# Optimization experiments

Hardware: AMD Instinct MI355X
Metric: run time of the kernel (lower is better)

## Reference

```python
import jax, jax.numpy as jnp
import numpy as np

N_NODES = 100000
N_EDGES = 3200000
N_GRAPHS = 256


def setup_inputs() -> dict:
    key = jax.random.key(0)
    ks = jax.random.split(key, 8)
    x = jax.random.normal(ks[0], (N_NODES, 13), dtype=jnp.float32)
    edge_index = jax.random.randint(ks[1], (2, N_EDGES), 0, N_NODES, dtype=jnp.int64)
    batch = jnp.sort(jax.random.randint(ks[2], (N_NODES,), 0, N_GRAPHS, dtype=jnp.int64))
    W1 = jax.random.normal(ks[3], (13, 64), dtype=jnp.float32) * 0.1
    b1 = jnp.zeros((64,), dtype=jnp.float32)
    W2 = jax.random.normal(ks[4], (64, 64), dtype=jnp.float32) * 0.1
    b2 = jnp.zeros((64,), dtype=jnp.float32)
    W3 = jax.random.normal(ks[5], (64, 32), dtype=jnp.float32) * 0.1
    b3 = jnp.zeros((32,), dtype=jnp.float32)
    return {"x": x, "edge_index": edge_index, "batch": batch,
            "W1": W1, "b1": b1, "W2": W2, "b2": b2, "W3": W3, "b3": b3}


def _gcn_norm(edge_index, num_nodes):
    # PyG GCNConv default: add self-loops, symmetric D^-1/2 (A+I) D^-1/2 normalization.
    loops = jnp.arange(num_nodes, dtype=edge_index.dtype)
    src = jnp.concatenate([edge_index[0], loops])
    dst = jnp.concatenate([edge_index[1], loops])
    ones = jnp.ones(src.shape[0], dtype=jnp.float32)
    deg = jax.ops.segment_sum(ones, dst, num_segments=num_nodes)
    dinv = jnp.where(deg > 0, jax.lax.rsqrt(deg), 0.0)
    norm = dinv[src] * dinv[dst]  # [E+N]
    return src, dst, norm


def _gcn_conv(h, W, b, src, dst, norm, num_nodes):
    h = h @ W                                   # [N, out]
    msg = h[src] * norm[:, None]                # gather + scale, [E+N, out]
    out = jax.ops.segment_sum(msg, dst, num_segments=num_nodes)  # scatter-add
    return out + b


def reference(x, edge_index, batch, W1, b1, W2, b2, W3, b3):
    n = x.shape[0]
    src, dst, norm = _gcn_norm(edge_index, n)
    h = jax.nn.relu(_gcn_conv(x, W1, b1, src, dst, norm, n))
    h = jax.nn.relu(_gcn_conv(h, W2, b2, src, dst, norm, n))
    h = _gcn_conv(h, W3, b3, src, dst, norm, n)
    # global_mean_pool over graphs
    sums = jax.ops.segment_sum(h, batch, num_segments=N_GRAPHS)
    counts = jax.ops.segment_sum(jnp.ones((n,), jnp.float32), batch, num_segments=N_GRAPHS)
    return sums / jnp.maximum(counts, 1.0)[:, None]
```

## Files before the change

### kernel.cpp

```cpp
#include <hip/hip_runtime.h>
#include <hip/hip_fp16.h>

constexpr int NN = 100000;
constexpr int NE = 3200000;
constexpr int NG = 256;
constexpr int NCB = 196;
constexpr int TILE = 4096;
constexpr int EPT = TILE / 256;
constexpr int CAP = 17408;

__global__ void k_zero_i(int* __restrict__ p, int n) {
  int i = blockIdx.x * blockDim.x + threadIdx.x;
  if (i < n) p[i] = 0;
}

__global__ void k_msplit(const int* __restrict__ src, const int* __restrict__ dst,
                         int* __restrict__ gcursor, int* __restrict__ pairs, int E) {
  constexpr int NT = 256;
  __shared__ int hist[NCB], lbase[NCB], lcur[NCB], gwrite[NCB];
  __shared__ int staged[TILE];
  __shared__ unsigned char sbid[TILE];
  __shared__ int stot;
  const int tid = threadIdx.x;
  const int e0 = blockIdx.x * TILE;
  for (int i = tid; i < NCB; i += NT) { hist[i] = 0; lcur[i] = 0; }
  __syncthreads();
  int4 ls[EPT / 4], ld[EPT / 4];
  bool valid[EPT / 4];
#pragma unroll
  for (int j = 0; j < EPT / 4; ++j) {
    int e = e0 + j * (NT * 4) + tid * 4;
    valid[j] = (e < E);
    if (valid[j]) {
      ls[j] = *(const int4*)(src + e);
      ld[j] = *(const int4*)(dst + e);
      atomicAdd(&hist[ld[j].x >> 9], 1);
      atomicAdd(&hist[ld[j].y >> 9], 1);
      atomicAdd(&hist[ld[j].z >> 9], 1);
      atomicAdd(&hist[ld[j].w >> 9], 1);
    }
  }
  __syncthreads();
  if (tid == 0) {
    int run = 0;
    for (int c = 0; c < NCB; ++c) { lbase[c] = run; run += hist[c]; }
    stot = run;
  }
  __syncthreads();
  for (int c = tid; c < NCB; c += NT) {
    int cnt = hist[c];
    if (cnt > 0) {
      int g = atomicAdd(&gcursor[c], cnt);
      gwrite[c] = c * CAP + g;
    }
  }
  __syncthreads();
#pragma unroll
  for (int j = 0; j < EPT / 4; ++j) {
    if (valid[j]) {
      int ss[4] = {ls[j].x, ls[j].y, ls[j].z, ls[j].w};
      int dd[4] = {ld[j].x, ld[j].y, ld[j].z, ld[j].w};
#pragma unroll
      for (int q = 0; q < 4; ++q) {
        int c = dd[q] >> 9;
        int pos = lbase[c] + atomicAdd(&lcur[c], 1);
        staged[pos] = ss[q] | ((dd[q] & 511) << 17);
        sbid[pos] = (unsigned char)c;
      }
    }
  }
  __syncthreads();
  const int total = stot;
  for (int i = tid; i < total; i += NT) {
    int c = sbid[i];
    pairs[gwrite[c] + (i - lbase[c])] = staged[i];
  }
}

__global__ void k_brow(const int* __restrict__ pairs, const int* __restrict__ gcursor,
                       int* __restrict__ rowstart, float* __restrict__ dinv,
                       int* __restrict__ csr_src) {
  __shared__ int deg[512], pre[512], cur[512];
  __shared__ int s[256];
  const int cb = blockIdx.x;
  const int n0 = cb << 9;
  const int tid = threadIdx.x;
  s[tid] = (tid < NCB) ? gcursor[tid] : 0;
  __syncthreads();
  for (int o = 1; o < 256; o <<= 1) {
    int v = s[tid];
    int u = (tid >= o) ? s[tid - o] : 0;
    __syncthreads();
    s[tid] = v + u;
    __syncthreads();
  }
  const int e0 = (cb == 0) ? 0 : s[cb - 1];
  const int cnt = gcursor[cb];
  const int p0 = cb * CAP;
  __syncthreads();
  for (int i = tid; i < 512; i += 256) { deg[i] = 0; cur[i] = 0; }
  __syncthreads();
  for (int e = tid; e < cnt; e += 256) atomicAdd(&deg[pairs[p0 + e] >> 17], 1);
  __syncthreads();
  int d0 = deg[2 * tid], d1 = deg[2 * tid + 1];
  s[tid] = d0 + d1;
  __syncthreads();
  for (int o = 1; o < 256; o <<= 1) {
    int v = s[tid];
    int u = (tid >= o) ? s[tid - o] : 0;
    __syncthreads();
    s[tid] = v + u;
    __syncthreads();
  }
  int p2 = (tid == 0) ? 0 : s[tid - 1];
  pre[2 * tid] = p2;
  pre[2 * tid + 1] = p2 + d0;
  __syncthreads();
  for (int i = tid; i < 512; i += 256) {
    int n = n0 + i;
    if (n < NN) {
      rowstart[n] = e0 + pre[i];
      dinv[n] = rsqrtf((float)(deg[i] + 1));
    }
  }
  if (cb == NCB - 1 && tid == 0) rowstart[NN] = NE;
  for (int e = tid; e < cnt; e += 256) {
    int w = pairs[p0 + e];
    int dl = w >> 17;
    int p = e0 + pre[dl] + atomicAdd(&cur[dl], 1);
    csr_src[p] = w & 0x1FFFF;
  }
}

__global__ void k_xs(const float* __restrict__ x, const float* __restrict__ dinv,
                     __half* __restrict__ xs) {
  int i = blockIdx.x * blockDim.x + threadIdx.x;
  if (i < NN * 16) {
    int v = i >> 4, f = i & 15;
    float val = (f < 13) ? x[v * 13 + f] * dinv[v] : 0.0f;
    xs[i] = __float2half_rn(val);
  }
}

__global__ void __launch_bounds__(256) k_l1fused(
    const __half* __restrict__ xs, const int* __restrict__ rowstart,
    const int* __restrict__ csr_src, const float* __restrict__ dinv,
    const float* __restrict__ W1, const float* __restrict__ b1,
    const float* __restrict__ W2, __half* __restrict__ t2) {
  __shared__ float W1s[13 * 64];
  __shared__ float B1s[64];
  __shared__ float W2s[64 * 64];
  __shared__ float aggs[4][16];
  __shared__ float h1s[4][64];
  __shared__ int lidx[4][64];
  const int tid = threadIdx.x;
  for (int i = tid; i < 13 * 64; i += 256) W1s[i] = W1[i];
  if (tid < 64) B1s[tid] = b1[tid];
  for (int i = tid; i < 64 * 64; i += 256) W2s[i] = W2[i];
  __syncthreads();
  const int wv = tid >> 6;
  const int lane = tid & 63;
  const int node = blockIdx.x * 4 + wv;
  const int fp = lane & 7;
  const int es = lane >> 3;
  const __half2* x2 = (const __half2*)xs;
  const int r0 = rowstart[node], r1 = rowstart[node + 1];
  float ax = 0.0f, ay = 0.0f;
  if (es == 0) {
    float2 sf = __half22float2(x2[node * 8 + fp]);
    ax = sf.x; ay = sf.y;
  }
  for (int base = r0; base < r1; base += 64) {
    const int nc = min(64, r1 - base);
    lidx[wv][lane] = (base + lane < r1) ? csr_src[base + lane] : 0;
    int i = es;
    for (; i + 24 < nc; i += 32) {
      int s0 = lidx[wv][i], s1 = lidx[wv][i + 8], s2 = lidx[wv][i + 16], s3 = lidx[wv][i + 24];
      float2 v0 = __half22float2(x2[s0 * 8 + fp]);
      float2 v1 = __half22float2(x2[s1 * 8 + fp]);
      float2 v2 = __half22float2(x2[s2 * 8 + fp]);
      float2 v3 = __half22float2(x2[s3 * 8 + fp]);
      ax += (v0.x + v1.x) + (v2.x + v3.x);
      ay += (v0.y + v1.y) + (v2.y + v3.y);
    }
    for (; i < nc; i += 8) {
      int s = lidx[wv][i];
      float2 v = __half22float2(x2[s * 8 + fp]);
      ax += v.x; ay += v.y;
    }
  }
  ax += __shfl_xor(ax, 32); ay += __shfl_xor(ay, 32);
  ax += __shfl_xor(ax, 16); ay += __shfl_xor(ay, 16);
  ax += __shfl_xor(ax, 8);  ay += __shfl_xor(ay, 8);
  const float di = dinv[node];
  if (lane < 8) {
    aggs[wv][2 * fp]     = ax * di;
    aggs[wv][2 * fp + 1] = ay * di;
  }
  float acc = B1s[lane];
#pragma unroll
  for (int k = 0; k < 13; ++k) acc += aggs[wv][k] * W1s[k * 64 + lane];
  h1s[wv][lane] = fmaxf(acc, 0.0f);
  float a2 = 0.0f;
#pragma unroll
  for (int k = 0; k < 64; ++k) a2 += h1s[wv][k] * W2s[k * 64 + lane];
  t2[node * 64 + lane] = __float2half_rn(a2 * di);
}

__global__ void __launch_bounds__(256) k_gather64m(
    const __half* __restrict__ t, const int* __restrict__ rowstart,
    const int* __restrict__ csr_src, const float* __restrict__ dinv,
    const float* __restrict__ b2, const float* __restrict__ W3,
    __half* __restrict__ t3) {
  __shared__ float W3s[64 * 32];
  __shared__ float h2s[4][64];
  __shared__ int lidx[4][64];
  const int tid = threadIdx.x;
  for (int i = tid; i < 64 * 32; i += 256) W3s[i] = W3[i];
  __syncthreads();
  const int w = tid >> 6;
  const int lane = tid & 63;
  const int node = blockIdx.x * 4 + w;
  const int fp = lane & 31;
  const int es = lane >> 5;
  const __half2* t2 = (const __half2*)t;
  const int r0 = rowstart[node], r1 = rowstart[node + 1];
  float ax = 0.0f, ay = 0.0f;
  if (es == 0) {
    float2 sf = __half22float2(t2[node * 32 + fp]);
    ax = sf.x; ay = sf.y;
  }
  for (int base = r0; base < r1; base += 64) {
    const int nc = min(64, r1 - base);
    lidx[w][lane] = (base + lane < r1) ? csr_src[base + lane] : 0;
    int i = es;
    for (; i + 14 < nc; i += 16) {
      int s0 = lidx[w][i],      s1 = lidx[w][i + 2],  s2 = lidx[w][i + 4],  s3 = lidx[w][i + 6];
      int s4 = lidx[w][i + 8],  s5 = lidx[w][i + 10], s6 = lidx[w][i + 12], s7 = lidx[w][i + 14];
      float2 v0 = __half22float2(t2[s0 * 32 + fp]);
      float2 v1 = __half22float2(t2[s1 * 32 + fp]);
      float2 v2 = __half22float2(t2[s2 * 32 + fp]);
      float2 v3 = __half22float2(t2[s3 * 32 + fp]);
      float2 v4 = __half22float2(t2[s4 * 32 + fp]);
      float2 v5 = __half22float2(t2[s5 * 32 + fp]);
      float2 v6 = __half22float2(t2[s6 * 32 + fp]);
      float2 v7 = __half22float2(t2[s7 * 32 + fp]);
      ax += ((v0.x + v1.x) + (v2.x + v3.x)) + ((v4.x + v5.x) + (v6.x + v7.x));
      ay += ((v0.y + v1.y) + (v2.y + v3.y)) + ((v4.y + v5.y) + (v6.y + v7.y));
    }
    for (; i < nc; i += 2) {
      int s = lidx[w][i];
      float2 v = __half22float2(t2[s * 32 + fp]);
      ax += v.x; ay += v.y;
    }
  }
  ax += __shfl_xor(ax, 32); ay += __shfl_xor(ay, 32);
  const float di = dinv[node];
  if (es == 0) {
    float2 bb = ((const float2*)b2)[fp];
    h2s[w][2 * fp]     = fmaxf(ax * di + bb.x, 0.0f);
    h2s[w][2 * fp + 1] = fmaxf(ay * di + bb.y, 0.0f);
  }
  const int j = lane & 31, kh = lane >> 5;
  float p = 0.0f;
#pragma unroll
  for (int k2 = 0; k2 < 32; ++k2) {
    int k = kh * 32 + k2;
    p += h2s[w][k] * W3s[k * 32 + j];
  }
  p += __shfl_xor(p, 32);
  if (lane < 32) t3[node * 32 + j] = __float2half_rn(p * di);
}

__global__ void k_gather32w(const __half* __restrict__ t, const int* __restrict__ rowstart,
                            const int* __restrict__ csr_src,
                            const float* __restrict__ dinv, const float* __restrict__ b,
                            __half* __restrict__ h3) {
  __shared__ int lidx[4][64];
  const int wv = threadIdx.x >> 6;
  const int node = (blockIdx.x * blockDim.x + threadIdx.x) >> 6;
  const int lane = threadIdx.x & 63;
  const int fp = lane & 15;
  const int es = lane >> 4;
  const __half2* t2 = (const __half2*)t;
  const int r0 = rowstart[node], r1 = rowstart[node + 1];
  float ax = 0.0f, ay = 0.0f;
  if (es == 0) {
    float2 sf = __half22float2(t2[node * 16 + fp]);
    ax = sf.x; ay = sf.y;
  }
  for (int base = r0; base < r1; base += 64) {
    const int nc = min(64, r1 - base);
    lidx[wv][lane] = (base + lane < r1) ? csr_src[base + lane] : 0;
    int i = es;
    for (; i + 28 < nc; i += 32) {
      int s0 = lidx[wv][i],      s1 = lidx[wv][i + 4],  s2 = lidx[wv][i + 8],  s3 = lidx[wv][i + 12];
      int s4 = lidx[wv][i + 16], s5 = lidx[wv][i + 20], s6 = lidx[wv][i + 24], s7 = lidx[wv][i + 28];
      float2 v0 = __half22float2(t2[s0 * 16 + fp]);
      float2 v1 = __half22float2(t2[s1 * 16 + fp]);
      float2 v2 = __half22float2(t2[s2 * 16 + fp]);
      float2 v3 = __half22float2(t2[s3 * 16 + fp]);
      float2 v4 = __half22float2(t2[s4 * 16 + fp]);
      float2 v5 = __half22float2(t2[s5 * 16 + fp]);
      float2 v6 = __half22float2(t2[s6 * 16 + fp]);
      float2 v7 = __half22float2(t2[s7 * 16 + fp]);
      ax += ((v0.x + v1.x) + (v2.x + v3.x)) + ((v4.x + v5.x) + (v6.x + v7.x));
      ay += ((v0.y + v1.y) + (v2.y + v3.y)) + ((v4.y + v5.y) + (v6.y + v7.y));
    }
    for (; i < nc; i += 4) {
      int s = lidx[wv][i];
      float2 v = __half22float2(t2[s * 16 + fp]);
      ax += v.x; ay += v.y;
    }
  }
  ax += __shfl_xor(ax, 32); ay += __shfl_xor(ay, 32);
  ax += __shfl_xor(ax, 16); ay += __shfl_xor(ay, 16);
  if (lane < 16) {
    const float di = dinv[node];
    float2 bb = ((const float2*)b)[fp];
    ((__half2*)h3)[node * 16 + fp] = __floats2half2_rn(ax * di + bb.x, ay * di + bb.y);
  }
}

__global__ void k_pool(const __half* __restrict__ h3, const int* __restrict__ batch,
                       float* __restrict__ out) {
  const int g = blockIdx.x;
  int lo = 0, hi = NN;
  while (lo < hi) { int m = (lo + hi) >> 1; if (batch[m] < g) lo = m + 1; else hi = m; }
  const int a = lo;
  lo = 0; hi = NN;
  while (lo < hi) { int m = (lo + hi) >> 1; if (batch[m] < g + 1) lo = m + 1; else hi = m; }
  const int bEnd = lo;
  const int tid = threadIdx.x;
  const int nl = tid >> 4, f = tid & 15;
  const __half2* h2p = (const __half2*)h3;
  float ax = 0.0f, ay = 0.0f;
  for (int n = a + nl; n < bEnd; n += 16) {
    float2 v = __half22float2(h2p[n * 16 + f]);
    ax += v.x; ay += v.y;
  }
  __shared__ float redx[16][16], redy[16][16];
  redx[nl][f] = ax; redy[nl][f] = ay;
  __syncthreads();
  if (tid < 16) {
    float sx = 0.0f, sy = 0.0f;
#pragma unroll
    for (int i = 0; i < 16; ++i) { sx += redx[i][tid]; sy += redy[i][tid]; }
    float inv = 1.0f / fmaxf((float)(bEnd - a), 1.0f);
    ((float2*)out)[g * 16 + tid] = make_float2(sx * inv, sy * inv);
  }
}

extern "C" void kernel_launch(void* const* d_in, const int* in_sizes, int n_in,
                              void* d_out, int out_size, void* d_ws, size_t ws_size,
                              hipStream_t stream) {
  const float* x  = (const float*)d_in[0];
  const int*   ei = (const int*)d_in[1];
  const int* batch = (const int*)d_in[2];
  const float* W1 = (const float*)d_in[3];
  const float* b1 = (const float*)d_in[4];
  const float* W2 = (const float*)d_in[5];
  const float* b2 = (const float*)d_in[6];
  const float* W3 = (const float*)d_in[7];
  const float* b3 = (const float*)d_in[8];
  float* out = (float*)d_out;

  const int* src = ei;
  const int* dst = ei + NE;

  float* ws = (float*)d_ws;
  float* dinv     = ws;
  int*   gcursor  = (int*)(ws + 100352);
  int*   rowstart = (int*)(ws + 100944);
  int*   csr_src  = (int*)(ws + 201056);
  float* bufT     = ws + 3401056;
  float* bufH     = ws + 9801056;
  int*    pairs = (int*)bufT;
  __half* t2    = (__half*)bufT;
  __half* h3    = (__half*)(bufT + 1600000);
  __half* xs    = (__half*)bufH;
  __half* t3    = (__half*)bufH;

  const int B = 256;
  auto cdiv = [](int a, int b) { return (a + b - 1) / b; };

  k_zero_i<<<1, B, 0, stream>>>(gcursor, NCB);
  k_msplit<<<cdiv(NE, TILE), B, 0, stream>>>(src, dst, gcursor, pairs, NE);
  k_brow<<<NCB, B, 0, stream>>>(pairs, gcursor, rowstart, dinv, csr_src);

  k_xs<<<cdiv(NN * 16, B), B, 0, stream>>>(x, dinv, xs);
  k_l1fused<<<NN / 4, B, 0, stream>>>(xs, rowstart, csr_src, dinv, W1, b1, W2, t2);

  k_gather64m<<<NN / 4, B, 0, stream>>>(t2, rowstart, csr_src, dinv, b2, W3, t3);

  k_gather32w<<<cdiv(NN * 64, B), B, 0, stream>>>(t3, rowstart, csr_src, dinv, b3, h3);
  k_pool<<<NG, B, 0, stream>>>(h3, batch, out);
}
```

Measured before the change: 319.9 us.

## Make layer-1 fused kernel persistent with W2 held in registers

The layer-1 gather+MLP kernel becomes a grid-stride persistent kernel with 1024 blocks instead of one block per 4 nodes. Each thread now keeps a 16x4 slice of W2 in registers, loaded once per block. The 64x64 matvec is split over four lane groups and reduced with cross-lane shuffles. This removes the per-block 16KB staging of W2 into shared memory repeated across 25000 blocks. The trade-off is higher register pressure, which may lower occupancy, and extra shuffle work per node.

```diff
diff --git a/kernel.cpp b/kernel.cpp
--- a/kernel.cpp
+++ b/kernel.cpp
@@ -8,6 +8,8 @@
 constexpr int TILE = 4096;
 constexpr int EPT = TILE / 256;
 constexpr int CAP = 17408;
+constexpr int L1_BLOCKS = 1024;
+constexpr int L1_WAVES = L1_BLOCKS * 4;
 
 __global__ void k_zero_i(int* __restrict__ p, int n) {
   int i = blockIdx.x * blockDim.x + threadIdx.x;
@@ -142,69 +144,89 @@
   }
 }
 
-__global__ void __launch_bounds__(256) k_l1fused(
+__global__ void __launch_bounds__(256, 4) k_l1fused(
     const __half* __restrict__ xs, const int* __restrict__ rowstart,
     const int* __restrict__ csr_src, const float* __restrict__ dinv,
     const float* __restrict__ W1, const float* __restrict__ b1,
     const float* __restrict__ W2, __half* __restrict__ t2) {
   __shared__ float W1s[13 * 64];
   __shared__ float B1s[64];
-  __shared__ float W2s[64 * 64];
   __shared__ float aggs[4][16];
   __shared__ float h1s[4][64];
   __shared__ int lidx[4][64];
   const int tid = threadIdx.x;
   for (int i = tid; i < 13 * 64; i += 256) W1s[i] = W1[i];
   if (tid < 64) B1s[tid] = b1[tid];
-  for (int i = tid; i < 64 * 64; i += 256) W2s[i] = W2[i];
-  __syncthreads();
   const int wv = tid >> 6;
   const int lane = tid & 63;
-  const int node = blockIdx.x * 4 + wv;
+  const int c4 = lane & 15, kh = lane >> 4;
+  float w2r[16][4];
+#pragma unroll
+  for (int i = 0; i < 16; ++i) {
+    float4 v = *(const float4*)(W2 + (kh * 16 + i) * 64 + c4 * 4);
+    w2r[i][0] = v.x; w2r[i][1] = v.y; w2r[i][2] = v.z; w2r[i][3] = v.w;
+  }
+  __syncthreads();
   const int fp = lane & 7;
   const int es = lane >> 3;
   const __half2* x2 = (const __half2*)xs;
-  const int r0 = rowstart[node], r1 = rowstart[node + 1];
-  float ax = 0.0f, ay = 0.0f;
-  if (es == 0) {
-    float2 sf = __half22float2(x2[node * 8 + fp]);
-    ax = sf.x; ay = sf.y;
-  }
-  for (int base = r0; base < r1; base += 64) {
-    const int nc = min(64, r1 - base);
-    lidx[wv][lane] = (base + lane < r1) ? csr_src[base + lane] : 0;
-    int i = es;
-    for (; i + 24 < nc; i += 32) {
-      int s0 = lidx[wv][i], s1 = lidx[wv][i + 8], s2 = lidx[wv][i + 16], s3 = lidx[wv][i + 24];
-      float2 v0 = __half22float2(x2[s0 * 8 + fp]);
-      float2 v1 = __half22float2(x2[s1 * 8 + fp]);
-      float2 v2 = __half22float2(x2[s2 * 8 + fp]);
-      float2 v3 = __half22float2(x2[s3 * 8 + fp]);
-      ax += (v0.x + v1.x) + (v2.x + v3.x);
-      ay += (v0.y + v1.y) + (v2.y + v3.y);
-    }
-    for (; i < nc; i += 8) {
-      int s = lidx[wv][i];
-      float2 v = __half22float2(x2[s * 8 + fp]);
-      ax += v.x; ay += v.y;
-    }
-  }
-  ax += __shfl_xor(ax, 32); ay += __shfl_xor(ay, 32);
-  ax += __shfl_xor(ax, 16); ay += __shfl_xor(ay, 16);
-  ax += __shfl_xor(ax, 8);  ay += __shfl_xor(ay, 8);
-  const float di = dinv[node];
-  if (lane < 8) {
-    aggs[wv][2 * fp]     = ax * di;
-    aggs[wv][2 * fp + 1] = ay * di;
-  }
-  float acc = B1s[lane];
-#pragma unroll
-  for (int k = 0; k < 13; ++k) acc += aggs[wv][k] * W1s[k * 64 + lane];
-  h1s[wv][lane] = fmaxf(acc, 0.0f);
-  float a2 = 0.0f;
-#pragma unroll
-  for (int k = 0; k < 64; ++k) a2 += h1s[wv][k] * W2s[k * 64 + lane];
-  t2[node * 64 + lane] = __float2half_rn(a2 * di);
+  for (int node = blockIdx.x * 4 + wv; node < NN; node += L1_WAVES) {
+    const int r0 = rowstart[node], r1 = rowstart[node + 1];
+    float ax = 0.0f, ay = 0.0f;
+    if (es == 0) {
+      float2 sf = __half22float2(x2[node * 8 + fp]);
+      ax = sf.x; ay = sf.y;
+    }
+    for (int base = r0; base < r1; base += 64) {
+      const int nc = min(64, r1 - base);
+      lidx[wv][lane] = (base + lane < r1) ? csr_src[base + lane] : 0;
+      int i = es;
+      for (; i + 24 < nc; i += 32) {
+        int s0 = lidx[wv][i], s1 = lidx[wv][i + 8], s2 = lidx[wv][i + 16], s3 = lidx[wv][i + 24];
+        float2 v0 = __half22float2(x2[s0 * 8 + fp]);
+        float2 v1 = __half22float2(x2[s1 * 8 + fp]);
+        float2 v2 = __half22float2(x2[s2 * 8 + fp]);
+        float2 v3 = __half22float2(x2[s3 * 8 + fp]);
+        ax += (v0.x + v1.x) + (v2.x + v3.x);
+        ay += (v0.y + v1.y) + (v2.y + v3.y);
+      }
+      for (; i < nc; i += 8) {
+        int s = lidx[wv][i];
+        float2 v = __half22float2(x2[s * 8 + fp]);
+        ax += v.x; ay += v.y;
+      }
+    }
+    ax += __shfl_xor(ax, 32); ay += __shfl_xor(ay, 32);
+    ax += __shfl_xor(ax, 16); ay += __shfl_xor(ay, 16);
+    ax += __shfl_xor(ax, 8);  ay += __shfl_xor(ay, 8);
+    const float di = dinv[node];
+    if (lane < 8) {
+      aggs[wv][2 * fp]     = ax * di;
+      aggs[wv][2 * fp + 1] = ay * di;
+    }
+    float acc = B1s[lane];
+#pragma unroll
+    for (int k = 0; k < 13; ++k) acc += aggs[wv][k] * W1s[k * 64 + lane];
+    h1s[wv][lane] = fmaxf(acc, 0.0f);
+    float a0 = 0.0f, a1 = 0.0f, a2 = 0.0f, a3 = 0.0f;
+#pragma unroll
+    for (int i = 0; i < 16; ++i) {
+      float hb = h1s[wv][kh * 16 + i];
+      a0 += hb * w2r[i][0];
+      a1 += hb * w2r[i][1];
+      a2 += hb * w2r[i][2];
+      a3 += hb * w2r[i][3];
+    }
+    a0 += __shfl_xor(a0, 16); a0 += __shfl_xor(a0, 32);
+    a1 += __shfl_xor(a1, 16); a1 += __shfl_xor(a1, 32);
+    a2 += __shfl_xor(a2, 16); a2 += __shfl_xor(a2, 32);
+    a3 += __shfl_xor(a3, 16); a3 += __shfl_xor(a3, 32);
+    if (kh == 0) {
+      __half2* o = (__half2*)t2;
+      o[node * 32 + c4 * 2]     = __floats2half2_rn(a0 * di, a1 * di);
+      o[node * 32 + c4 * 2 + 1] = __floats2half2_rn(a2 * di, a3 * di);
+    }
+  }
 }
 
 __global__ void __launch_bounds__(256) k_gather64m(
@@ -389,7 +411,7 @@
   k_brow<<<NCB, B, 0, stream>>>(pairs, gcursor, rowstart, dinv, csr_src);
 
   k_xs<<<cdiv(NN * 16, B), B, 0, stream>>>(x, dinv, xs);
-  k_l1fused<<<NN / 4, B, 0, stream>>>(xs, rowstart, csr_src, dinv, W1, b1, W2, t2);
+  k_l1fused<<<L1_BLOCKS, B, 0, stream>>>(xs, rowstart, csr_src, dinv, W1, b1, W2, t2);
 
   k_gather64m<<<NN / 4, B, 0, stream>>>(t2, rowstart, csr_src, dinv, b2, W3, t3);
 
```

Measured after the change: 295.2 us. 7.7% less time.
